# Kernel tuning notes

Hardware: AMD Instinct MI355X
Metric: run time of the kernel (lower is better)

Reference implementation:

```python
import jax, jax.numpy as jnp
import numpy as np

NEG_SLOPE = 0.2  # PyG GATConv leaky_relu slope
EPS = 1e-16


def gat_layer(x, W, att_src, att_dst, bias, src, dst, num_nodes, heads, out_c, concat):
    # x: [N, F_in], W: [F_in, heads*out_c], att_*: [heads, out_c], bias: [heads*out_c] or [out_c]
    xp = (x @ W).reshape(num_nodes, heads, out_c)              # [N, H, C]
    a_src = (xp * att_src).sum(-1)                             # [N, H]
    a_dst = (xp * att_dst).sum(-1)                             # [N, H]
    alpha = jax.nn.leaky_relu(a_src[src] + a_dst[dst], NEG_SLOPE)  # [E, H]
    # segment softmax over destination-node neighborhoods
    m = jax.ops.segment_max(alpha, dst, num_segments=num_nodes)   # [N, H]
    e = jnp.exp(alpha - m[dst])
    s = jax.ops.segment_sum(e, dst, num_segments=num_nodes)
    alpha = e / (s[dst] + EPS)                                 # [E, H]
    out = jax.ops.segment_sum(xp[src] * alpha[:, :, None], dst, num_segments=num_nodes)  # [N, H, C]
    out = out.reshape(num_nodes, heads * out_c) if concat else out.mean(axis=1)
    return out + bias


def setup_inputs() -> dict:
    key = jax.random.key(0)
    N, E, F = 100000, 3200000, 128
    ks = jax.random.split(key, 10)
    x = jax.random.normal(ks[0], (N, F), dtype=jnp.float32)
    edge_index = jax.random.randint(ks[1], (2, E), 0, N, dtype=jnp.int64)
    s1 = 1.0 / np.sqrt(F)
    W1 = jax.random.normal(ks[2], (F, 2 * 16), dtype=jnp.float32) * s1
    att_src1 = jax.random.normal(ks[3], (2, 16), dtype=jnp.float32) * 0.25
    att_dst1 = jax.random.normal(ks[4], (2, 16), dtype=jnp.float32) * 0.25
    b1 = jnp.zeros((32,), dtype=jnp.float32)
    W2 = jax.random.normal(ks[5], (32, 1), dtype=jnp.float32) * (1.0 / np.sqrt(32))
    att_src2 = jax.random.normal(ks[6], (1, 1), dtype=jnp.float32)
    att_dst2 = jax.random.normal(ks[7], (1, 1), dtype=jnp.float32)
    b2 = jnp.zeros((1,), dtype=jnp.float32)
    return {"x": x, "edge_index": edge_index, "W1": W1, "att_src1": att_src1,
            "att_dst1": att_dst1, "b1": b1, "W2": W2, "att_src2": att_src2,
            "att_dst2": att_dst2, "b2": b2}


def reference(x, edge_index, W1, att_src1, att_dst1, b1, W2, att_src2, att_dst2, b2):
    N = x.shape[0]
    # PyG GATConv adds self-loops by default
    loops = jnp.arange(N, dtype=edge_index.dtype)
    src = jnp.concatenate([edge_index[0], loops])
    dst = jnp.concatenate([edge_index[1], loops])
    h = gat_layer(x, W1, att_src1, att_dst1, b1, src, dst, N, 2, 16, True)   # [N, 32]
    h = jax.nn.relu(h)
    out = gat_layer(h, W2, att_src2, att_dst2, b2, src, dst, N, 1, 1, False)  # [N, 1]
    return out.sum(axis=0, keepdims=True)  # [1, 1]
```

## Files before the change

### kernel.cpp

```cpp
#include <hip/hip_runtime.h>
#include <hip/hip_bf16.h>
#include <hip/hip_fp16.h>
#include <hip/hip_fp8.h>
#include <math.h>

#define NEG_SLOPE 0.2f
#define EPS 1e-16f
#define CHUNK 4096
#define BSH 8
#define BNODES 256

__device__ __forceinline__ float leaky(float x) {
    return x > 0.f ? x : NEG_SLOPE * x;
}

__global__ __launch_bounds__(1024) void chunkhist_kernel(
    const int* __restrict__ ei, int E, int ET, int NB, int NC,
    int* __restrict__ cnt) {
    __shared__ int histL[1024];
    int t = threadIdx.x;
    int c = blockIdx.x;
    if (t < NB) histL[t] = 0;
    __syncthreads();
    int e0 = c * CHUNK;
#pragma unroll 4
    for (int i = t; i < CHUNK; i += 1024) {
        int e = e0 + i;
        if (e < ET) {
            int d = (e < E) ? ei[E + e] : (e - E);
            atomicAdd(&histL[d >> BSH], 1);
        }
    }
    __syncthreads();
    if (t < NB) cnt[(size_t)t * NC + c] = histL[t];
}

__global__ void scan_block(const int* __restrict__ in, int* __restrict__ out,
                           int* __restrict__ partials, int n) {
    __shared__ int tmp[1024];
    int t = threadIdx.x;
    int g = blockIdx.x * 1024 + t;
    int v = (g < n) ? in[g] : 0;
    tmp[t] = v;
    __syncthreads();
    for (int off = 1; off < 1024; off <<= 1) {
        int add = (t >= off) ? tmp[t - off] : 0;
        __syncthreads();
        tmp[t] += add;
        __syncthreads();
    }
    if (g < n) out[g] = tmp[t] - v;
    if (t == 1023) partials[blockIdx.x] = tmp[1023];
}

__global__ void scan_partials(int* __restrict__ partials, int P) {
    __shared__ int tmp[1024];
    int t = threadIdx.x;
    int v = (t < P) ? partials[t] : 0;
    tmp[t] = v;
    __syncthreads();
    for (int off = 1; off < 1024; off <<= 1) {
        int add = (t >= off) ? tmp[t - off] : 0;
        __syncthreads();
        tmp[t] += add;
        __syncthreads();
    }
    if (t < P) partials[t] = tmp[t] - v;
}

__device__ __forceinline__ int gscan(const int* scanned, const int* partials,
                                     size_t g) {
    return scanned[g] + partials[g >> 10];
}

__global__ __launch_bounds__(1024) void packsort_kernel(
    const int* __restrict__ ei, int E, int ET, int NB, int NC,
    const int* __restrict__ scanned, const int* __restrict__ partials,
    unsigned int* __restrict__ packed) {
    __shared__ unsigned int sortedL[CHUNK];
    __shared__ int gposL[CHUNK];
    __shared__ int histL[1024];
    __shared__ int tmpL[1024];
    __shared__ int cursorL[1024];
    __shared__ int diffL[1024];
    int t = threadIdx.x;
    int c = blockIdx.x;
    int e0 = c * CHUNK;
    int cw = ET - e0; if (cw > CHUNK) cw = CHUNK;

    if (t < NB) histL[t] = 0;
    __syncthreads();

    unsigned int pk[4]; int bb[4];
#pragma unroll
    for (int k = 0; k < 4; k++) {
        int i = t + k * 1024;
        bb[k] = -1;
        if (i < cw) {
            int e = e0 + i;
            int s, d;
            if (e < E) { s = ei[e]; d = ei[E + e]; } else { s = d = e - E; }
            bb[k] = d >> BSH;
            pk[k] = ((unsigned int)s << BSH) | (unsigned int)(d & (BNODES - 1));
            atomicAdd(&histL[bb[k]], 1);
        }
    }
    __syncthreads();
    int hv = (t < NB) ? histL[t] : 0;
    tmpL[t] = hv;
    __syncthreads();
    for (int off = 1; off < 1024; off <<= 1) {
        int add = (t >= off) ? tmpL[t - off] : 0;
        __syncthreads();
        tmpL[t] += add;
        __syncthreads();
    }
    if (t < NB) {
        int loff = tmpL[t] - hv;
        cursorL[t] = loff;
        size_t g = (size_t)t * NC + c;
        diffL[t] = gscan(scanned, partials, g) - loff;
    }
    __syncthreads();
#pragma unroll
    for (int k = 0; k < 4; k++) {
        if (bb[k] >= 0) {
            int lpos = atomicAdd(&cursorL[bb[k]], 1);
            sortedL[lpos] = pk[k];
            gposL[lpos] = diffL[bb[k]] + lpos;
        }
    }
    __syncthreads();
    for (int i = t; i < cw; i += 1024)
        packed[gposL[i]] = sortedL[i];
}

__global__ __launch_bounds__(1024) void localsort_kernel(
    const unsigned int* __restrict__ packed, const int* __restrict__ scanned,
    const int* __restrict__ partials, int NB, int NC, int ET,
    int* __restrict__ srt, int* __restrict__ binptr, int N) {
    __shared__ int histL[BNODES];
    __shared__ int offL[BNODES];
    __shared__ int curL[BNODES];
    int t = threadIdx.x;
    int bkt = blockIdx.x;
    int base = bkt * BNODES;
    int ebeg = gscan(scanned, partials, (size_t)bkt * NC);
    int eend = (bkt + 1 < NB) ? gscan(scanned, partials, (size_t)(bkt + 1) * NC) : ET;
    if (t < BNODES) histL[t] = 0;
    __syncthreads();
    for (int i = ebeg + t; i < eend; i += 1024)
        atomicAdd(&histL[packed[i] & (BNODES - 1)], 1);
    __syncthreads();
    if (t < BNODES) offL[t] = histL[t];
    __syncthreads();
    for (int off = 1; off < BNODES; off <<= 1) {
        int add = (t >= off && t < BNODES) ? offL[t - off] : 0;
        __syncthreads();
        if (t < BNODES) offL[t] += add;
        __syncthreads();
    }
    if (t < BNODES) {
        int ex = offL[t] - histL[t];
        curL[t] = ex;
        int gn = base + t;
        if (gn < N) binptr[gn] = ebeg + ex;
    }
    if (bkt == 0 && t == 0) binptr[N] = ET;
    __syncthreads();
    for (int i = ebeg + t; i < eend; i += 1024) {
        unsigned int p = packed[i];
        int dl = p & (BNODES - 1);
        int pos = ebeg + atomicAdd(&curL[dl], 1);
        srt[pos] = (int)(p >> BSH);
    }
}

__device__ __forceinline__ void fma4(float4& acc, float sc, const float4& wv) {
    acc.x = fmaf(sc, wv.x, acc.x);
    acc.y = fmaf(sc, wv.y, acc.y);
    acc.z = fmaf(sc, wv.z, acc.z);
    acc.w = fmaf(sc, wv.w, acc.w);
}

__global__ __launch_bounds__(256) void gemm1_kernel(
    const float* __restrict__ x, const float* __restrict__ W1,
    const float4* __restrict__ att_src4, const float4* __restrict__ att_dst4,
    unsigned int* __restrict__ xp1u, float* __restrict__ a_src,
    float* __restrict__ a_dst, int N) {
    __shared__ float4 wS4[128 * 8];
    __shared__ float4 xS4[64 * 32];
    int t = threadIdx.x;
    int base = blockIdx.x * 64;
#pragma unroll
    for (int i = 0; i < 4; i++)
        wS4[t + i * 256] = ((const float4*)W1)[t + i * 256];
#pragma unroll
    for (int i = 0; i < 8; i++) {
        int idx = t + i * 256;
        int row = idx >> 5, kb = idx & 31;
        xS4[idx] = (base + row < N) ? ((const float4*)x)[(size_t)(base + row) * 32 + kb]
                                    : make_float4(0.f, 0.f, 0.f, 0.f);
    }
    __syncthreads();

    int cq = t & 7;
    int rg = t >> 3;
    const float4* xr0 = xS4 + (rg * 2) * 32;
    const float4* xr1 = xr0 + 32;
    float4 a0 = make_float4(0.f, 0.f, 0.f, 0.f);
    float4 a1 = make_float4(0.f, 0.f, 0.f, 0.f);
#pragma unroll 4
    for (int kb = 0; kb < 32; kb++) {
        float4 x0 = xr0[kb];
        float4 x1 = xr1[kb];
        float4 w0 = wS4[(kb * 4 + 0) * 8 + cq];
        float4 w1 = wS4[(kb * 4 + 1) * 8 + cq];
        float4 w2 = wS4[(kb * 4 + 2) * 8 + cq];
        float4 w3 = wS4[(kb * 4 + 3) * 8 + cq];
        fma4(a0, x0.x, w0); fma4(a0, x0.y, w1); fma4(a0, x0.z, w2); fma4(a0, x0.w, w3);
        fma4(a1, x1.x, w0); fma4(a1, x1.y, w1); fma4(a1, x1.z, w2); fma4(a1, x1.w, w3);
    }

    float4 asv = att_src4[cq];
    float4 adv = att_dst4[cq];
    int r0 = base + rg * 2, r1 = r0 + 1;
    float va0 = a0.x * asv.x + a0.y * asv.y + a0.z * asv.z + a0.w * asv.w;
    float vd0 = a0.x * adv.x + a0.y * adv.y + a0.z * adv.z + a0.w * adv.w;
    float va1 = a1.x * asv.x + a1.y * asv.y + a1.z * asv.z + a1.w * asv.w;
    float vd1 = a1.x * adv.x + a1.y * adv.y + a1.z * adv.z + a1.w * adv.w;
#pragma unroll
    for (int off = 1; off <= 2; off <<= 1) {
        va0 += __shfl_xor(va0, off);
        vd0 += __shfl_xor(vd0, off);
        va1 += __shfl_xor(va1, off);
        vd1 += __shfl_xor(vd1, off);
    }
    if (r0 < N) {
        __hip_fp8x4_e4m3 q0(a0);
        xp1u[(size_t)r0 * 8 + cq] = *(unsigned int*)&q0;
        if ((cq & 3) == 0) {
            int h = cq >> 2;
            a_src[r0 * 2 + h] = va0;
            a_dst[r0 * 2 + h] = vd0;
        }
    }
    if (r1 < N) {
        __hip_fp8x4_e4m3 q1(a1);
        xp1u[(size_t)r1 * 8 + cq] = *(unsigned int*)&q1;
        if ((cq & 3) == 0) {
            int h = cq >> 2;
            a_src[r1 * 2 + h] = va1;
            a_dst[r1 * 2 + h] = vd1;
        }
    }
}

#define AGG1_CONSUME(KN)                                                        \
    _Pragma("unroll")                                                           \
    for (int k = 0; k < KN; k++) {                                              \
        int es = k * 8 + eg;                                                    \
        int sk = __shfl(s_l, es);                                               \
        unsigned int pw = (unsigned int)__shfl((int)pk_l, es);                  \
        float ek = __uint_as_float(hsel ? (pw & 0xFFFF0000u) : (pw << 16));     \
        unsigned int u = *(const unsigned int*)(xpb + (size_t)sk * 32);         \
        float4 xv = (float4)(*reinterpret_cast<const __hip_fp8x4_e4m3*>(&u));   \
        acc0 = fmaf(ek, xv.x, acc0);                                            \
        acc1 = fmaf(ek, xv.y, acc1);                                            \
        acc2 = fmaf(ek, xv.z, acc2);                                            \
        acc3 = fmaf(ek, xv.w, acc3);                                            \
        ssum += ek;                                                             \
    }

__global__ __launch_bounds__(256) void agg1_kernel(
    const int* __restrict__ binptr, const int* __restrict__ srt,
    const float2* __restrict__ a_src2, const float2* __restrict__ a_dst2,
    const unsigned char* __restrict__ xp1f8, const float* __restrict__ b1,
    const float* __restrict__ W2, float* __restrict__ xp2, int N) {
    int tg = blockIdx.x * blockDim.x + threadIdx.x;
    int n = tg >> 6;
    int lane = threadIdx.x & 63;
    if (n >= N) return;
    int eg = lane >> 3;
    int cq = lane & 7;
    int hsel = cq >> 2;
    int beg = binptr[n], end = binptr[n + 1];
    float2 ad = a_dst2[n];
    const unsigned char* xpb = xp1f8 + cq * 4;

    float acc0 = 0.f, acc1 = 0.f, acc2 = 0.f, acc3 = 0.f, ssum = 0.f;
    for (int i0 = beg; i0 < end; i0 += 64) {
        int cw = end - i0;
        if (cw > 64) cw = 64;
        int s_l = 0;
        unsigned int pk_l = 0u;
        if (lane < cw) {
            s_l = srt[i0 + lane];
            float2 as = a_src2[s_l];
            float e0 = __expf(leaky(as.x + ad.x));
            float e1 = __expf(leaky(as.y + ad.y));
            pk_l = ((__float_as_uint(e1) + 0x8000u) & 0xFFFF0000u) |
                   ((__float_as_uint(e0) + 0x8000u) >> 16);
        }
        if (cw > 48)      { AGG1_CONSUME(8) }
        else if (cw > 32) { AGG1_CONSUME(6) }
        else if (cw > 16) { AGG1_CONSUME(4) }
        else              { AGG1_CONSUME(2) }
    }
#pragma unroll
    for (int off = 8; off <= 32; off <<= 1) {
        acc0 += __shfl_xor(acc0, off);
        acc1 += __shfl_xor(acc1, off);
        acc2 += __shfl_xor(acc2, off);
        acc3 += __shfl_xor(acc3, off);
        ssum += __shfl_xor(ssum, off);
    }
    float inv = 1.f / (ssum + EPS);
    int j0 = cq * 4;
    float p;
    {
        float hv0 = fmaxf(acc0 * inv + b1[j0 + 0], 0.f);
        float hv1 = fmaxf(acc1 * inv + b1[j0 + 1], 0.f);
        float hv2 = fmaxf(acc2 * inv + b1[j0 + 2], 0.f);
        float hv3 = fmaxf(acc3 * inv + b1[j0 + 3], 0.f);
        p = hv0 * W2[j0 + 0];
        p = fmaf(hv1, W2[j0 + 1], p);
        p = fmaf(hv2, W2[j0 + 2], p);
        p = fmaf(hv3, W2[j0 + 3], p);
    }
    p += __shfl_xor(p, 1);
    p += __shfl_xor(p, 2);
    p += __shfl_xor(p, 4);
    if (lane == 0) xp2[n] = p;
}

__global__ __launch_bounds__(256) void agg2_kernel(
    const int* __restrict__ binptr, const int* __restrict__ srt,
    const float* __restrict__ xp2, const float* __restrict__ as2p,
    const float* __restrict__ ad2p, const float* __restrict__ b2,
    float* __restrict__ partial, int N) {
    int slot = (blockIdx.x * blockDim.x + threadIdx.x) >> 5;
    int j = threadIdx.x & 31;
    int nslots = (gridDim.x * blockDim.x) >> 5;
    float as2 = as2p[0], ad2 = ad2p[0], bb = b2[0];
    float val = 0.f;
    for (int n = slot; n < N; n += nslots) {
        int beg = binptr[n], end = binptr[n + 1];
        float xd = xp2[n] * ad2;
        float se = 0.f, sa = 0.f;
        for (int i = beg + j; i < end; i += 32) {
            float xs = xp2[srt[i]];
            float ex = __expf(leaky(fmaf(xs, as2, xd)));
            se += ex;
            sa = fmaf(ex, xs, sa);
        }
#pragma unroll
        for (int off = 16; off >= 1; off >>= 1) {
            se += __shfl_xor(se, off);
            sa += __shfl_xor(sa, off);
        }
        if (j == 0) val += sa / (se + EPS) + bb;
    }
#pragma unroll
    for (int off = 32; off >= 1; off >>= 1) val += __shfl_xor(val, off);
    __shared__ float ls[4];
    int lane = threadIdx.x & 63, w = threadIdx.x >> 6;
    if (lane == 0) ls[w] = val;
    __syncthreads();
    if (threadIdx.x == 0) partial[blockIdx.x] = ls[0] + ls[1] + ls[2] + ls[3];
}

__global__ void final_reduce(const float* __restrict__ partial, float* __restrict__ out,
                             int P) {
    int t = threadIdx.x;
    float v = 0.f;
    for (int i = t; i < P; i += 1024) v += partial[i];
#pragma unroll
    for (int off = 32; off >= 1; off >>= 1) v += __shfl_xor(v, off);
    __shared__ float ls[16];
    int w = t >> 6, lane = t & 63;
    if (lane == 0) ls[w] = v;
    __syncthreads();
    if (t == 0) {
        float s = 0.f;
        for (int i = 0; i < 16; i++) s += ls[i];
        out[0] = s;
    }
}

extern "C" void kernel_launch(void* const* d_in, const int* in_sizes, int n_in,
                              void* d_out, int out_size, void* d_ws, size_t ws_size,
                              hipStream_t stream) {
    const float* x        = (const float*)d_in[0];
    const int*   ei       = (const int*)d_in[1];
    const float* W1       = (const float*)d_in[2];
    const float* att_src1 = (const float*)d_in[3];
    const float* att_dst1 = (const float*)d_in[4];
    const float* b1       = (const float*)d_in[5];
    const float* W2       = (const float*)d_in[6];
    const float* att_src2 = (const float*)d_in[7];
    const float* att_dst2 = (const float*)d_in[8];
    const float* b2       = (const float*)d_in[9];
    float* out = (float*)d_out;

    int N = in_sizes[0] / 128;
    int E = in_sizes[1] / 2;
    int ET = E + N;
    int NB = (N + BNODES - 1) / BNODES;
    int NC = (ET + CHUNK - 1) / CHUNK;
    int n_scan = NB * NC;
    int nb2 = (n_scan + 1023) / 1024;
    const int AGG2_BLOCKS = 2048;

    char* w = (char*)d_ws;
    unsigned char* xp1f8 = (unsigned char*)w; w += (size_t)N * 32;
    float* a_src   = (float*)w;  w += sizeof(float) * (size_t)N * 2;
    float* a_dst   = (float*)w;  w += sizeof(float) * (size_t)N * 2;
    float* xp2     = (float*)w;  w += sizeof(float) * (size_t)N;
    int* cnt       = (int*)w;    w += sizeof(int) * (size_t)n_scan;
    int* scanned   = (int*)w;    w += sizeof(int) * (size_t)(n_scan + 4);
    int* partials  = (int*)w;    w += sizeof(int) * 1024;
    float* part2   = (float*)w;  w += sizeof(float) * (size_t)AGG2_BLOCKS;
    unsigned int* packed = (unsigned int*)w; w += sizeof(unsigned int) * (size_t)ET;
    int* srt       = (int*)w;    w += sizeof(int) * (size_t)ET;
    int* binptr    = (int*)w;    w += sizeof(int) * (size_t)(N + 1);

    gemm1_kernel<<<(N + 63) / 64, 256, 0, stream>>>(x, W1,
                                                    (const float4*)att_src1,
                                                    (const float4*)att_dst1,
                                                    (unsigned int*)xp1f8, a_src,
                                                    a_dst, N);
    chunkhist_kernel<<<NC, 1024, 0, stream>>>(ei, E, ET, NB, NC, cnt);
    scan_block<<<nb2, 1024, 0, stream>>>(cnt, scanned, partials, n_scan);
    scan_partials<<<1, 1024, 0, stream>>>(partials, nb2);
    packsort_kernel<<<NC, 1024, 0, stream>>>(ei, E, ET, NB, NC, scanned, partials,
                                             packed);
    localsort_kernel<<<NB, 1024, 0, stream>>>(packed, scanned, partials, NB, NC, ET,
                                              srt, binptr, N);
    agg1_kernel<<<(N * 64 + 255) / 256, 256, 0, stream>>>(binptr, srt,
                                                          (const float2*)a_src,
                                                          (const float2*)a_dst,
                                                          xp1f8, b1, W2, xp2, N);
    agg2_kernel<<<AGG2_BLOCKS, 256, 0, stream>>>(binptr, srt, xp2,
                                                 att_src2, att_dst2, b2, part2, N);
    final_reduce<<<1, 1024, 0, stream>>>(part2, out, AGG2_BLOCKS);
}
```

Before: 155.8 us.

## Use wave-shuffle block scans and LDS staging of edge weights in agg1

Replaces the Hillis-Steele shared-memory scans, which need 20 barriers each, with a wave-level shuffle scan plus a small cross-wave pass in the scan, packsort and localsort kernels. In agg1, per-edge source index and exp weights are staged in LDS as float4 instead of being broadcast with two shuffles per edge. This also drops the bf16 packing of the weights, keeping full fp32 precision. The agg1 staging relies on wave-synchronous execution without a barrier, and the broadcast LDS reads replace cross-lane shuffles.

```diff
diff --git a/kernel.cpp b/kernel.cpp
--- a/kernel.cpp
+++ b/kernel.cpp
@@ -12,6 +12,30 @@
 
 __device__ __forceinline__ float leaky(float x) {
     return x > 0.f ? x : NEG_SLOPE * x;
+}
+
+__device__ __forceinline__ int block_scan_excl_1024(int v, int t, int* waveS) {
+    int lane = t & 63, w = t >> 6;
+    int inc = v;
+#pragma unroll
+    for (int off = 1; off < 64; off <<= 1) {
+        int u = __shfl_up(inc, off);
+        if (lane >= off) inc += u;
+    }
+    if (lane == 63) waveS[w] = inc;
+    __syncthreads();
+    if (w == 0) {
+        int s = (lane < 16) ? waveS[lane] : 0;
+#pragma unroll
+        for (int off = 1; off < 16; off <<= 1) {
+            int u = __shfl_up(s, off);
+            if (lane >= off) s += u;
+        }
+        if (lane < 16) waveS[lane] = s;
+    }
+    __syncthreads();
+    int base = (w > 0) ? waveS[w - 1] : 0;
+    return base + inc - v;
 }
 
 __global__ __launch_bounds__(1024) void chunkhist_kernel(
@@ -37,35 +61,21 @@
 
 __global__ void scan_block(const int* __restrict__ in, int* __restrict__ out,
                            int* __restrict__ partials, int n) {
-    __shared__ int tmp[1024];
+    __shared__ int waveS[16];
     int t = threadIdx.x;
     int g = blockIdx.x * 1024 + t;
     int v = (g < n) ? in[g] : 0;
-    tmp[t] = v;
-    __syncthreads();
-    for (int off = 1; off < 1024; off <<= 1) {
-        int add = (t >= off) ? tmp[t - off] : 0;
-        __syncthreads();
-        tmp[t] += add;
-        __syncthreads();
-    }
-    if (g < n) out[g] = tmp[t] - v;
-    if (t == 1023) partials[blockIdx.x] = tmp[1023];
+    int ex = block_scan_excl_1024(v, t, waveS);
+    if (g < n) out[g] = ex;
+    if (t == 0) partials[blockIdx.x] = waveS[15];
 }
 
 __global__ void scan_partials(int* __restrict__ partials, int P) {
-    __shared__ int tmp[1024];
+    __shared__ int waveS[16];
     int t = threadIdx.x;
     int v = (t < P) ? partials[t] : 0;
-    tmp[t] = v;
-    __syncthreads();
-    for (int off = 1; off < 1024; off <<= 1) {
-        int add = (t >= off) ? tmp[t - off] : 0;
-        __syncthreads();
-        tmp[t] += add;
-        __syncthreads();
-    }
-    if (t < P) partials[t] = tmp[t] - v;
+    int ex = block_scan_excl_1024(v, t, waveS);
+    if (t < P) partials[t] = ex;
 }
 
 __device__ __forceinline__ int gscan(const int* scanned, const int* partials,
@@ -80,9 +90,9 @@
     __shared__ unsigned int sortedL[CHUNK];
     __shared__ int gposL[CHUNK];
     __shared__ int histL[1024];
-    __shared__ int tmpL[1024];
     __shared__ int cursorL[1024];
     __shared__ int diffL[1024];
+    __shared__ int waveS[16];
     int t = threadIdx.x;
     int c = blockIdx.x;
     int e0 = c * CHUNK;
@@ -107,19 +117,11 @@
     }
     __syncthreads();
     int hv = (t < NB) ? histL[t] : 0;
-    tmpL[t] = hv;
-    __syncthreads();
-    for (int off = 1; off < 1024; off <<= 1) {
-        int add = (t >= off) ? tmpL[t - off] : 0;
-        __syncthreads();
-        tmpL[t] += add;
-        __syncthreads();
-    }
+    int ex = block_scan_excl_1024(hv, t, waveS);
     if (t < NB) {
-        int loff = tmpL[t] - hv;
-        cursorL[t] = loff;
+        cursorL[t] = ex;
         size_t g = (size_t)t * NC + c;
-        diffL[t] = gscan(scanned, partials, g) - loff;
+        diffL[t] = gscan(scanned, partials, g) - ex;
     }
     __syncthreads();
 #pragma unroll
@@ -140,8 +142,8 @@
     const int* __restrict__ partials, int NB, int NC, int ET,
     int* __restrict__ srt, int* __restrict__ binptr, int N) {
     __shared__ int histL[BNODES];
-    __shared__ int offL[BNODES];
     __shared__ int curL[BNODES];
+    __shared__ int waveS[16];
     int t = threadIdx.x;
     int bkt = blockIdx.x;
     int base = bkt * BNODES;
@@ -152,16 +154,9 @@
     for (int i = ebeg + t; i < eend; i += 1024)
         atomicAdd(&histL[packed[i] & (BNODES - 1)], 1);
     __syncthreads();
-    if (t < BNODES) offL[t] = histL[t];
-    __syncthreads();
-    for (int off = 1; off < BNODES; off <<= 1) {
-        int add = (t >= off && t < BNODES) ? offL[t - off] : 0;
-        __syncthreads();
-        if (t < BNODES) offL[t] += add;
-        __syncthreads();
-    }
+    int hv = (t < BNODES) ? histL[t] : 0;
+    int ex = block_scan_excl_1024(hv, t, waveS);
     if (t < BNODES) {
-        int ex = offL[t] - histL[t];
         curL[t] = ex;
         int gn = base + t;
         if (gn < N) binptr[gn] = ebeg + ex;
@@ -259,10 +254,9 @@
 #define AGG1_CONSUME(KN)                                                        \
     _Pragma("unroll")                                                           \
     for (int k = 0; k < KN; k++) {                                              \
-        int es = k * 8 + eg;                                                    \
-        int sk = __shfl(s_l, es);                                               \
-        unsigned int pw = (unsigned int)__shfl((int)pk_l, es);                  \
-        float ek = __uint_as_float(hsel ? (pw & 0xFFFF0000u) : (pw << 16));     \
+        float4 st = stage[wib][k * 8 + eg];                                     \
+        int sk = __float_as_int(st.x);                                          \
+        float ek = hsel ? st.z : st.y;                                          \
         unsigned int u = *(const unsigned int*)(xpb + (size_t)sk * 32);         \
         float4 xv = (float4)(*reinterpret_cast<const __hip_fp8x4_e4m3*>(&u));   \
         acc0 = fmaf(ek, xv.x, acc0);                                            \
@@ -277,9 +271,11 @@
     const float2* __restrict__ a_src2, const float2* __restrict__ a_dst2,
     const unsigned char* __restrict__ xp1f8, const float* __restrict__ b1,
     const float* __restrict__ W2, float* __restrict__ xp2, int N) {
+    __shared__ float4 stage[4][64];
     int tg = blockIdx.x * blockDim.x + threadIdx.x;
     int n = tg >> 6;
     int lane = threadIdx.x & 63;
+    int wib = threadIdx.x >> 6;
     if (n >= N) return;
     int eg = lane >> 3;
     int cq = lane & 7;
@@ -292,15 +288,14 @@
     for (int i0 = beg; i0 < end; i0 += 64) {
         int cw = end - i0;
         if (cw > 64) cw = 64;
-        int s_l = 0;
-        unsigned int pk_l = 0u;
         if (lane < cw) {
-            s_l = srt[i0 + lane];
+            int s_l = srt[i0 + lane];
             float2 as = a_src2[s_l];
-            float e0 = __expf(leaky(as.x + ad.x));
-            float e1 = __expf(leaky(as.y + ad.y));
-            pk_l = ((__float_as_uint(e1) + 0x8000u) & 0xFFFF0000u) |
-                   ((__float_as_uint(e0) + 0x8000u) >> 16);
+            stage[wib][lane] = make_float4(__int_as_float(s_l),
+                                           __expf(leaky(as.x + ad.x)),
+                                           __expf(leaky(as.y + ad.y)), 0.f);
+        } else {
+            stage[wib][lane] = make_float4(0.f, 0.f, 0.f, 0.f);
         }
         if (cw > 48)      { AGG1_CONSUME(8) }
         else if (cw > 32) { AGG1_CONSUME(6) }
```

Measured after the change: 154.5 us. No clear change (-0.9%).
